# Performance work log

Hardware: AMD Instinct MI355X
Metric: run time of the kernel (lower is better)

Reference implementation:

```python
import jax, jax.numpy as jnp
import numpy as np

# dims: batch B, seq T, model C, expert hidden H, num experts E, top-k K
B, T, C, H, E, K = 4, 1024, 1024, 1024, 8, 2


def _swiglu(x):
    a, b = jnp.split(x, 2, axis=-1)
    return jax.nn.silu(a) * b


def setup_inputs() -> dict:
    key = jax.random.key(0)
    ks = jax.random.split(key, 6)
    s = 0.02
    x = jax.random.normal(ks[0], (B, T, C), jnp.float32)
    # weights stored [in, out] (transpose of torch Linear layout; same math y = x @ W)
    w_shared_in = jax.random.normal(ks[1], (C, 2 * H), jnp.float32) * s
    w_shared_out = jax.random.normal(ks[2], (H, C), jnp.float32) * s
    w1_shared = jax.random.normal(ks[3], (C, 2 * H), jnp.float32) * s
    w2 = jax.random.normal(ks[4], (E, H, C), jnp.float32) * s  # stacked routed_w2
    w_gate = jax.random.normal(ks[5], (C, E), jnp.float32) * s
    gate_bias = jnp.zeros((E,), jnp.float32)  # buffer, updated only in training
    return {
        "x": x,
        "w_shared_in": w_shared_in,
        "w_shared_out": w_shared_out,
        "w1_shared": w1_shared,
        "w2": w2,
        "w_gate": w_gate,
        "gate_bias": gate_bias,
    }


def reference(x, w_shared_in, w_shared_out, w1_shared, w2, w_gate, gate_bias):
    Bx, Tx, Cx = x.shape
    S = Bx * Tx
    fx = x.reshape(S, Cx)  # [S, C]

    # shared expert: SwiGLU MLP
    shared_out = _swiglu(fx @ w_shared_in) @ w_shared_out  # [S, C]

    # router: softmax(top-k) over biased logits
    logits = fx @ w_gate + gate_bias  # [S, E]
    probs = jax.nn.softmax(logits, axis=-1)
    top_val, top_idx = jax.lax.top_k(probs, K)  # [S, K]

    # dense dispatch-weight matrix [S, E] (zero where expert not selected)
    wdense = jnp.zeros((S, E), probs.dtype).at[
        jnp.arange(S)[:, None], top_idx
    ].add(top_val)

    # routed experts share w1_shared, so the SwiGLU hidden is identical for all
    # experts; compute it once for every token, then apply per-expert w2.
    hid = _swiglu(fx @ w1_shared)  # [S, H]
    routed_out = jnp.zeros_like(shared_out)
    for e in range(E):  # small fixed expert count
        routed_out = routed_out + wdense[:, e:e + 1] * (hid @ w2[e])

    return (shared_out + routed_out).reshape(Bx, Tx, Cx)
```

## Files before the change

kernel.cpp:

```cpp
#include <hip/hip_runtime.h>
#include <stdint.h>

typedef __attribute__((ext_vector_type(4))) float f32x4;
typedef __attribute__((ext_vector_type(8))) short s16x8;

static constexpr int S_TOK = 4096;
static constexpr int CDIM  = 1024;
static constexpr int HDIM  = 1024;
static constexpr int H2    = 2048;
static constexpr int NEXP  = 8;

#define BK 32
#define MAXRT2 40

__device__ __forceinline__ unsigned short f2bf(float f) {
  union { float f; uint32_t u; } c; c.f = f;
  uint32_t u = c.u;
  u += 0x7fffu + ((u >> 16) & 1u);
  return (unsigned short)(u >> 16);
}

__device__ __forceinline__ float bf2f(unsigned short u) {
  return __uint_as_float(((uint32_t)u) << 16);
}

__device__ __forceinline__ void gload16(const void* g, void* l) {
  __builtin_amdgcn_global_load_lds(
      (const __attribute__((address_space(1))) void*)g,
      (__attribute__((address_space(3))) void*)l, 16, 0, 0);
}

__global__ void cast_bf16_kernel(const float* __restrict__ src,
                                 unsigned short* __restrict__ dst, int n4) {
  int i = blockIdx.x * blockDim.x + threadIdx.x;
  const int st = gridDim.x * blockDim.x;
  for (; i < n4; i += st) {
    float4 v = reinterpret_cast<const float4*>(src)[i];
    ushort4 o;
    o.x = f2bf(v.x); o.y = f2bf(v.y); o.z = f2bf(v.z); o.w = f2bf(v.w);
    reinterpret_cast<ushort4*>(dst)[i] = o;
  }
}

__global__ void wprep_in_kernel(const float* __restrict__ wsi, const float* __restrict__ w1s,
                                unsigned short* __restrict__ dst) {
  __shared__ float t[32][33];
  const float* src = blockIdx.z ? w1s : wsi;
  const int halfoff = blockIdx.z ? 2048 : 0;
  const int r0 = blockIdx.y * 32;
  const int c0 = blockIdx.x * 32;
  const int tid = threadIdx.x;
#pragma unroll
  for (int i = 0; i < 4; ++i) {
    int idx = tid + i * 256;
    int r = idx >> 5, c = idx & 31;
    t[r][c] = src[(size_t)(r0 + r) * H2 + c0 + c];
  }
  __syncthreads();
#pragma unroll
  for (int i = 0; i < 4; ++i) {
    int idx = tid + i * 256;
    int r = idx >> 5, c = idx & 31;
    const int ccol = c0 + r;
    const int part = ccol >> 10, h = ccol & 1023;
    const int drow = halfoff + (h & 15) + ((h >> 4) << 5) + (part << 4);
    dst[(size_t)drow * CDIM + r0 + c] = f2bf(t[c][r]);
  }
}

__global__ void transpose_cast_kernel(const float* __restrict__ src,
                                      unsigned short* __restrict__ dst,
                                      int R, int Cc) {
  __shared__ float t[32][33];
  const size_t zoff = (size_t)blockIdx.z * R * Cc;
  src += zoff; dst += zoff;
  const int r0 = blockIdx.y * 32;
  const int c0 = blockIdx.x * 32;
  const int tid = threadIdx.x;
#pragma unroll
  for (int i = 0; i < 4; ++i) {
    int idx = tid + i * 256;
    int r = idx >> 5, c = idx & 31;
    t[r][c] = src[(size_t)(r0 + r) * Cc + c0 + c];
  }
  __syncthreads();
#pragma unroll
  for (int i = 0; i < 4; ++i) {
    int idx = tid + i * 256;
    int r = idx >> 5, c = idx & 31;
    dst[(size_t)(c0 + r) * R + r0 + c] = f2bf(t[c][r]);
  }
}

__global__ void router_kernel(const float* __restrict__ x, const float* __restrict__ wg,
                              const float* __restrict__ gb,
                              int2* __restrict__ ti_e, float2* __restrict__ ti_w) {
  const int l = threadIdx.x & 63;
  const int wid = threadIdx.x >> 6;
  const int s = blockIdx.x * 4 + wid;
  const float* xr = x + (size_t)s * CDIM;
  float acc[NEXP];
#pragma unroll
  for (int e = 0; e < NEXP; ++e) acc[e] = 0.f;
  for (int c = l; c < CDIM; c += 64) {
    float xv = xr[c];
    const float* wr_ = wg + (size_t)c * NEXP;
#pragma unroll
    for (int e = 0; e < NEXP; ++e) acc[e] += xv * wr_[e];
  }
#pragma unroll
  for (int e = 0; e < NEXP; ++e) {
#pragma unroll
    for (int off = 32; off > 0; off >>= 1) acc[e] += __shfl_xor(acc[e], off);
    acc[e] += gb[e];
  }
  float m = acc[0];
#pragma unroll
  for (int e = 1; e < NEXP; ++e) m = fmaxf(m, acc[e]);
  float ex[NEXP], sum = 0.f;
#pragma unroll
  for (int e = 0; e < NEXP; ++e) { ex[e] = __expf(acc[e] - m); sum += ex[e]; }
  int i0 = 0;
#pragma unroll
  for (int e = 1; e < NEXP; ++e) if (acc[e] > acc[i0]) i0 = e;
  int i1 = (i0 == 0) ? 1 : 0;
#pragma unroll
  for (int e = 0; e < NEXP; ++e) {
    if (e == i0) continue;
    if (acc[e] > acc[i1]) i1 = e;
  }
  if (l == 0) {
    const float inv = 1.f / sum;
    ti_e[s] = make_int2(i0, i1);
    ti_w[s] = make_float2(ex[i0] * inv, ex[i1] * inv);
  }
}

__global__ __launch_bounds__(1024) void build_kernel(
    const int2* __restrict__ ti_e,
    int* __restrict__ cnt, int* __restrict__ offs,
    int* __restrict__ gidx, int2* __restrict__ ti_slot) {
  __shared__ int gcnt[64][NEXP];
  __shared__ int gbase[64][NEXP];
  __shared__ int eoff[NEXP];
  const int tid = threadIdx.x;
  const int wid = tid >> 6, lane = tid & 63;

  for (int p = 0; p < 4; ++p) {
    const int g = p * 16 + wid;
    const int2 e = ti_e[g * 64 + lane];
#pragma unroll
    for (int ex = 0; ex < NEXP; ++ex) {
      uint64_t b0 = __ballot(e.x == ex);
      uint64_t b1 = __ballot(e.y == ex);
      if (lane == 0) gcnt[g][ex] = __popcll(b0) + __popcll(b1);
    }
  }
  __syncthreads();
  if (tid < NEXP) {
    const int ex = tid;
    int a = 0;
    for (int g = 0; g < 64; ++g) { gbase[g][ex] = a; a += gcnt[g][ex]; }
    eoff[ex] = a;
  }
  __syncthreads();
  if (tid == 0) {
    int a = 0;
#pragma unroll
    for (int ex = 0; ex < NEXP; ++ex) {
      const int c = eoff[ex];
      offs[ex] = a; cnt[ex] = c; eoff[ex] = a; a += c;
    }
    offs[NEXP] = a;
  }
  __syncthreads();
  for (int p = 0; p < 4; ++p) {
    const int g = p * 16 + wid;
    const int s = g * 64 + lane;
    const int2 e = ti_e[s];
    const uint64_t below = (lane == 0) ? 0ull : (~0ull >> (64 - lane));
    const uint64_t beloweq = below | (1ull << lane);
    int slot0 = 0, slot1 = 0;
#pragma unroll
    for (int ex = 0; ex < NEXP; ++ex) {
      uint64_t b0 = __ballot(e.x == ex);
      uint64_t b1 = __ballot(e.y == ex);
      const int base = gbase[g][ex];
      if (e.x == ex) slot0 = base + __popcll(b0 & below) + __popcll(b1 & below);
      if (e.y == ex) slot1 = base + __popcll(b0 & beloweq) + __popcll(b1 & below);
    }
    ti_slot[s] = make_int2(slot0, slot1);
    gidx[eoff[e.x] + slot0] = s;
    gidx[eoff[e.y] + slot1] = s;
  }
}

__global__ __launch_bounds__(256, 4) void gemm1_kernel(
    const unsigned short* __restrict__ xb, const unsigned short* __restrict__ w12i,
    unsigned short* __restrict__ Hs, unsigned short* __restrict__ Hr) {
  __shared__ unsigned short As[128 * BK];
  __shared__ unsigned short Bs[128 * BK];
  const int tid = threadIdx.x;
  const int l = tid & 63, wid = tid >> 6;
  const int wr = wid >> 1, wc = wid & 1;
  const int lr = l & 15, lk = (l >> 4) << 3;
  const int hw = blockIdx.y * gridDim.x + blockIdx.x;
  const int logical = (hw & 7) * 128 + (hw >> 3);
  const int m0 = (logical >> 5) * 128;
  const int n0 = (logical & 31) * 128;
  f32x4 acc[4][4] = {};
  const unsigned short* ga0 = xb + (size_t)(m0 + (tid >> 2)) * CDIM + ((tid & 3) << 3);
  const unsigned short* ga1 = ga0 + (size_t)64 * CDIM;
  const unsigned short* gb0 = w12i + (size_t)(n0 + (tid >> 2)) * CDIM + ((tid & 3) << 3);
  const unsigned short* gb1 = gb0 + (size_t)64 * CDIM;

  for (int k0 = 0; k0 < 1024; k0 += BK) {
    gload16(ga0 + k0, As + tid * 8);
    gload16(ga1 + k0, As + 2048 + tid * 8);
    gload16(gb0 + k0, Bs + tid * 8);
    gload16(gb1 + k0, Bs + 2048 + tid * 8);
    __syncthreads();
    s16x8 a[4], b[4];
#pragma unroll
    for (int fm = 0; fm < 4; ++fm)
      a[fm] = *reinterpret_cast<const s16x8*>(As + (wr * 64 + fm * 16 + lr) * BK + lk);
#pragma unroll
    for (int fn = 0; fn < 4; ++fn)
      b[fn] = *reinterpret_cast<const s16x8*>(Bs + (wc * 64 + fn * 16 + lr) * BK + lk);
#pragma unroll
    for (int fm = 0; fm < 4; ++fm)
#pragma unroll
      for (int fn = 0; fn < 4; ++fn)
        acc[fm][fn] = __builtin_amdgcn_mfma_f32_16x16x32_bf16(a[fm], b[fn], acc[fm][fn], 0, 0, 0);
    __syncthreads();
  }

  unsigned short* Hbuf = (n0 < 2048) ? Hs : Hr;
  const int rb = m0 + wr * 64 + ((l >> 4) << 2);
  const int hb0 = ((n0 & 2047) >> 1) + wc * 32;
#pragma unroll
  for (int fm = 0; fm < 4; ++fm)
#pragma unroll
    for (int j = 0; j < 2; ++j)
#pragma unroll
      for (int r = 0; r < 4; ++r) {
        float a = acc[fm][2 * j][r];
        float b = acc[fm][2 * j + 1][r];
        float hv = (a / (1.f + __expf(-a))) * b;
        Hbuf[(size_t)(rb + fm * 16 + r) * HDIM + hb0 + j * 16 + lr] = f2bf(hv);
      }
}

__global__ __launch_bounds__(512) void gemm2_kernel(
    const unsigned short* __restrict__ Hs, const unsigned short* __restrict__ Hr,
    const unsigned short* __restrict__ wso_t, const unsigned short* __restrict__ w2t,
    const int* __restrict__ cnt, const int* __restrict__ offs, const int* __restrict__ gidx,
    float* __restrict__ out, unsigned short* __restrict__ Eout) {
  __shared__ unsigned short As[2][256 * BK];
  __shared__ unsigned short Bs[2][256 * BK];
  const int tid = threadIdx.x;
  const int l = tid & 63, wid = tid >> 6;
  const int wm = wid >> 2, wn = wid & 3;
  const int lr = l & 15, lk = (l >> 4) << 3;
  const int hw = blockIdx.y * gridDim.x + blockIdx.x;
  const int logical = (hw & 7) * 28 + (hw >> 3);
  const int gx = logical >> 2;
  const int n0 = (logical & 3) * 256;
  f32x4 acc[8][4] = {};

  const int srow = tid >> 2, scol = (tid & 3) << 3;

  const unsigned short* ga0;
  const unsigned short* ga1;
  const unsigned short* gb0;
  const unsigned short* gb1;
  int e = 0, cnte = 0, mt = 0, base = 0;
  const bool dense = (gx < 16);
  if (dense) {
    const int m0 = gx * 256;
    ga0 = Hs + (size_t)(m0 + srow) * HDIM + scol;
    ga1 = ga0 + (size_t)128 * HDIM;
    gb0 = wso_t + (size_t)(n0 + srow) * HDIM + scol;
    gb1 = gb0 + (size_t)128 * HDIM;
  } else {
    int t = gx - 16;
    bool found = false;
#pragma unroll
    for (int ee = 0; ee < NEXP; ++ee) {
      int c = cnt[ee];
      int nt = (c + 255) >> 8;
      if (!found) {
        if (t < nt) { e = ee; cnte = c; found = true; }
        else t -= nt;
      }
    }
    if (!found) return;
    mt = t;
    base = offs[e];
    const int g0 = mt * 256 + srow;
    const int g1 = g0 + 128;
    const int tok0 = gidx[base + min(g0, cnte - 1)];
    const int tok1 = gidx[base + min(g1, cnte - 1)];
    ga0 = Hr + (size_t)tok0 * HDIM + scol;
    ga1 = Hr + (size_t)tok1 * HDIM + scol;
    gb0 = w2t + (size_t)e * CDIM * HDIM + (size_t)(n0 + srow) * HDIM + scol;
    gb1 = gb0 + (size_t)128 * HDIM;
  }

#define STG2(buf, k0) do { \
    gload16(ga0 + (k0), As[buf] + tid * 8); \
    gload16(ga1 + (k0), As[buf] + 4096 + tid * 8); \
    gload16(gb0 + (k0), Bs[buf] + tid * 8); \
    gload16(gb1 + (k0), Bs[buf] + 4096 + tid * 8); \
  } while (0)

  STG2(0, 0);
  asm volatile("s_waitcnt vmcnt(0)" ::: "memory");
  __builtin_amdgcn_s_barrier();
  asm volatile("" ::: "memory");

  const int NT = 1024 / BK;
  for (int t = 0; t < NT; ++t) {
    const int cur = t & 1;
    if (t + 1 < NT) STG2(cur ^ 1, (t + 1) * BK);
    const unsigned short* Ac = As[cur];
    const unsigned short* Bc = Bs[cur];
    s16x8 a[8], b[4];
#pragma unroll
    for (int fm = 0; fm < 8; ++fm)
      a[fm] = *reinterpret_cast<const s16x8*>(Ac + (wm * 128 + fm * 16 + lr) * BK + lk);
#pragma unroll
    for (int fn = 0; fn < 4; ++fn)
      b[fn] = *reinterpret_cast<const s16x8*>(Bc + (wn * 64 + fn * 16 + lr) * BK + lk);
    __builtin_amdgcn_s_setprio(1);
#pragma unroll
    for (int fm = 0; fm < 8; ++fm)
#pragma unroll
      for (int fn = 0; fn < 4; ++fn)
        acc[fm][fn] = __builtin_amdgcn_mfma_f32_16x16x32_bf16(a[fm], b[fn], acc[fm][fn], 0, 0, 0);
    __builtin_amdgcn_s_setprio(0);
    if (t + 1 < NT) {
      asm volatile("s_waitcnt vmcnt(0)" ::: "memory");
      __builtin_amdgcn_s_barrier();
      asm volatile("" ::: "memory");
    }
  }
#undef STG2

  const int rloc0 = wm * 128 + ((l >> 4) << 2);
  const int cb = n0 + wn * 64 + lr;
  if (dense) {
    const int rb = gx * 256 + rloc0;
#pragma unroll
    for (int fm = 0; fm < 8; ++fm)
#pragma unroll
      for (int fn = 0; fn < 4; ++fn)
#pragma unroll
        for (int r = 0; r < 4; ++r)
          out[(size_t)(rb + fm * 16 + r) * CDIM + cb + fn * 16] = acc[fm][fn][r];
  } else {
#pragma unroll
    for (int fm = 0; fm < 8; ++fm)
#pragma unroll
      for (int fn = 0; fn < 4; ++fn)
#pragma unroll
        for (int r = 0; r < 4; ++r) {
          const int rloc = mt * 256 + rloc0 + fm * 16 + r;
          if (rloc < cnte)
            Eout[(size_t)(base + rloc) * CDIM + cb + fn * 16] = f2bf(acc[fm][fn][r]);
        }
  }
}

__global__ void scatter_kernel(float* __restrict__ out, const unsigned short* __restrict__ Eout,
                               const int2* __restrict__ ti_e, const int2* __restrict__ ti_slot,
                               const float2* __restrict__ ti_w, const int* __restrict__ offs) {
  const int total = S_TOK * (CDIM / 8);
  int i = blockIdx.x * blockDim.x + threadIdx.x;
  const int st = gridDim.x * blockDim.x;
  for (; i < total; i += st) {
    const int s = i >> 7;
    const int j = (i & 127) << 3;
    const int2 e = ti_e[s];
    const int2 sl = ti_slot[s];
    const float2 wv = ti_w[s];
    const int p0 = offs[e.x] + sl.x;
    const int p1 = offs[e.y] + sl.y;
    const ushort4* e0 = reinterpret_cast<const ushort4*>(Eout + (size_t)p0 * CDIM + j);
    const ushort4* e1 = reinterpret_cast<const ushort4*>(Eout + (size_t)p1 * CDIM + j);
    float* op = out + (size_t)s * CDIM + j;
#pragma unroll
    for (int q = 0; q < 2; ++q) {
      ushort4 a = e0[q], b = e1[q];
      float4 o = reinterpret_cast<float4*>(op)[q];
      o.x += wv.x * bf2f(a.x) + wv.y * bf2f(b.x);
      o.y += wv.x * bf2f(a.y) + wv.y * bf2f(b.y);
      o.z += wv.x * bf2f(a.z) + wv.y * bf2f(b.z);
      o.w += wv.x * bf2f(a.w) + wv.y * bf2f(b.w);
      reinterpret_cast<float4*>(op)[q] = o;
    }
  }
}

extern "C" void kernel_launch(void* const* d_in, const int* in_sizes, int n_in,
                              void* d_out, int out_size, void* d_ws, size_t ws_size,
                              hipStream_t stream) {
  (void)in_sizes; (void)n_in; (void)out_size; (void)ws_size;
  const float* x   = (const float*)d_in[0];
  const float* wsi = (const float*)d_in[1];
  const float* wso = (const float*)d_in[2];
  const float* w1s = (const float*)d_in[3];
  const float* w2  = (const float*)d_in[4];
  const float* wg  = (const float*)d_in[5];
  const float* gb  = (const float*)d_in[6];
  float* out = (float*)d_out;

  char* w = (char*)d_ws;
  auto alloc = [&](size_t bytes) {
    char* p = w; w += (bytes + 255) & ~(size_t)255; return p;
  };
  unsigned short* xb    = (unsigned short*)alloc((size_t)S_TOK * CDIM * 2);
  unsigned short* w12i  = (unsigned short*)alloc((size_t)2 * H2 * CDIM * 2);
  unsigned short* wso_t = (unsigned short*)alloc((size_t)CDIM * HDIM * 2);
  unsigned short* w2t   = (unsigned short*)alloc((size_t)NEXP * CDIM * HDIM * 2);
  unsigned short* Hs    = (unsigned short*)alloc((size_t)S_TOK * HDIM * 2);
  unsigned short* Hr    = (unsigned short*)alloc((size_t)S_TOK * HDIM * 2);
  unsigned short* Eout  = (unsigned short*)alloc((size_t)2 * S_TOK * CDIM * 2);
  int2*   ti_e   = (int2*)alloc((size_t)S_TOK * 8);
  int2*   ti_slot= (int2*)alloc((size_t)S_TOK * 8);
  float2* ti_w   = (float2*)alloc((size_t)S_TOK * 8);
  int*    cnt    = (int*)alloc(64);
  int*    offs   = (int*)alloc(64);
  int*    gidx   = (int*)alloc((size_t)2 * S_TOK * 4);

  router_kernel<<<S_TOK / 4, 256, 0, stream>>>(x, wg, gb, ti_e, ti_w);
  build_kernel<<<1, 1024, 0, stream>>>(ti_e, cnt, offs, gidx, ti_slot);

  cast_bf16_kernel<<<2048, 256, 0, stream>>>(x, xb, S_TOK * CDIM / 4);
  wprep_in_kernel<<<dim3(H2 / 32, CDIM / 32, 2), 256, 0, stream>>>(wsi, w1s, w12i);
  transpose_cast_kernel<<<dim3(CDIM / 32, HDIM / 32, 1), 256, 0, stream>>>(wso, wso_t, HDIM, CDIM);
  transpose_cast_kernel<<<dim3(CDIM / 32, HDIM / 32, NEXP), 256, 0, stream>>>(w2, w2t, HDIM, CDIM);

  gemm1_kernel<<<dim3(32, 32), 256, 0, stream>>>(xb, w12i, Hs, Hr);

  gemm2_kernel<<<dim3(16 + MAXRT2, CDIM / 256), 512, 0, stream>>>(
      Hs, Hr, wso_t, w2t, cnt, offs, gidx, out, Eout);

  scatter_kernel<<<2048, 256, 0, stream>>>(out, Eout, ti_e, ti_slot, ti_w, offs);
}
```

Baseline: 139.7 us.

## Deepen gemm2 pipeline to 4-stage ring with swizzled LDS and interleaved loads

Replaces gemm2's double-buffered K loop with a 4-slot LDS ring, keeping three stages of global-to-LDS loads in flight and waiting with partial vmcnt counts instead of draining to zero. The per-stage global loads are spread between four MFMA sub-blocks. An XOR swizzle is applied to the LDS column index on both store and read to reduce bank conflicts. The aim is to hide memory latency and cut per-iteration barrier stalls, at the cost of doubling shared memory, which may reduce occupancy.

```diff
diff --git a/kernel.cpp b/kernel.cpp
--- a/kernel.cpp
+++ b/kernel.cpp
@@ -256,32 +256,33 @@
     const unsigned short* __restrict__ wso_t, const unsigned short* __restrict__ w2t,
     const int* __restrict__ cnt, const int* __restrict__ offs, const int* __restrict__ gidx,
     float* __restrict__ out, unsigned short* __restrict__ Eout) {
-  __shared__ unsigned short As[2][256 * BK];
-  __shared__ unsigned short Bs[2][256 * BK];
+  __shared__ unsigned short SA[4][2][4096];
+  __shared__ unsigned short SB[4][2][4096];
   const int tid = threadIdx.x;
   const int l = tid & 63, wid = tid >> 6;
   const int wm = wid >> 2, wn = wid & 3;
-  const int lr = l & 15, lk = (l >> 4) << 3;
+  const int lr = l & 15;
+  const int hi8 = (l >> 4) << 3;
+  const int wnh = wn >> 1;
+  const int wno = (wn & 1) << 6;
   const int hw = blockIdx.y * gridDim.x + blockIdx.x;
   const int logical = (hw & 7) * 28 + (hw >> 3);
   const int gx = logical >> 2;
   const int n0 = (logical & 3) * 256;
   f32x4 acc[8][4] = {};
 
-  const int srow = tid >> 2, scol = (tid & 3) << 3;
-
-  const unsigned short* ga0;
-  const unsigned short* ga1;
-  const unsigned short* gb0;
-  const unsigned short* gb1;
+  const int srow = tid >> 2;
+  const int cs = (((tid & 3) ^ ((tid >> 3) & 3)) << 3);
+
+  const unsigned short *pa0, *pa1, *pb0, *pb1;
   int e = 0, cnte = 0, mt = 0, base = 0;
   const bool dense = (gx < 16);
   if (dense) {
     const int m0 = gx * 256;
-    ga0 = Hs + (size_t)(m0 + srow) * HDIM + scol;
-    ga1 = ga0 + (size_t)128 * HDIM;
-    gb0 = wso_t + (size_t)(n0 + srow) * HDIM + scol;
-    gb1 = gb0 + (size_t)128 * HDIM;
+    pa0 = Hs + (size_t)(m0 + srow) * HDIM + cs;
+    pa1 = pa0 + (size_t)128 * HDIM;
+    pb0 = wso_t + (size_t)(n0 + srow) * HDIM + cs;
+    pb1 = pb0 + (size_t)128 * HDIM;
   } else {
     int t = gx - 16;
     bool found = false;
@@ -297,55 +298,81 @@
     if (!found) return;
     mt = t;
     base = offs[e];
-    const int g0 = mt * 256 + srow;
-    const int g1 = g0 + 128;
-    const int tok0 = gidx[base + min(g0, cnte - 1)];
-    const int tok1 = gidx[base + min(g1, cnte - 1)];
-    ga0 = Hr + (size_t)tok0 * HDIM + scol;
-    ga1 = Hr + (size_t)tok1 * HDIM + scol;
-    gb0 = w2t + (size_t)e * CDIM * HDIM + (size_t)(n0 + srow) * HDIM + scol;
-    gb1 = gb0 + (size_t)128 * HDIM;
-  }
-
-#define STG2(buf, k0) do { \
-    gload16(ga0 + (k0), As[buf] + tid * 8); \
-    gload16(ga1 + (k0), As[buf] + 4096 + tid * 8); \
-    gload16(gb0 + (k0), Bs[buf] + tid * 8); \
-    gload16(gb1 + (k0), Bs[buf] + 4096 + tid * 8); \
-  } while (0)
-
-  STG2(0, 0);
-  asm volatile("s_waitcnt vmcnt(0)" ::: "memory");
-  __builtin_amdgcn_s_barrier();
-  asm volatile("" ::: "memory");
-
-  const int NT = 1024 / BK;
-  for (int t = 0; t < NT; ++t) {
-    const int cur = t & 1;
-    if (t + 1 < NT) STG2(cur ^ 1, (t + 1) * BK);
-    const unsigned short* Ac = As[cur];
-    const unsigned short* Bc = Bs[cur];
+    const int r0 = mt * 256 + srow;
+    const int tok0 = gidx[base + min(r0, cnte - 1)];
+    const int tok1 = gidx[base + min(r0 + 128, cnte - 1)];
+    pa0 = Hr + (size_t)tok0 * HDIM + cs;
+    pa1 = Hr + (size_t)tok1 * HDIM + cs;
+    pb0 = w2t + (size_t)e * CDIM * HDIM + (size_t)(n0 + srow) * HDIM + cs;
+    pb1 = pb0 + (size_t)128 * HDIM;
+  }
+
+  const int t8 = tid * 8;
+#pragma unroll
+  for (int s = 0; s < 3; ++s) {
+    const int kk = s * 32;
+    gload16(pa0 + kk, &SA[s][0][t8]);
+    gload16(pa1 + kk, &SA[s][1][t8]);
+    gload16(pb0 + kk, &SB[s][0][t8]);
+    gload16(pb1 + kk, &SB[s][1][t8]);
+  }
+
+  for (int s = 0; s < 32; ++s) {
+    if (s < 30)       asm volatile("s_waitcnt vmcnt(8)" ::: "memory");
+    else if (s == 30) asm volatile("s_waitcnt vmcnt(4)" ::: "memory");
+    else              asm volatile("s_waitcnt vmcnt(0)" ::: "memory");
+    __builtin_amdgcn_s_barrier();
+    asm volatile("" ::: "memory");
+    const int c = s & 3;
+    const unsigned short* A_ = &SA[c][wm][0];
+    const unsigned short* B_ = &SB[c][wnh][0];
     s16x8 a[8], b[4];
 #pragma unroll
-    for (int fm = 0; fm < 8; ++fm)
-      a[fm] = *reinterpret_cast<const s16x8*>(Ac + (wm * 128 + fm * 16 + lr) * BK + lk);
-#pragma unroll
-    for (int fn = 0; fn < 4; ++fn)
-      b[fn] = *reinterpret_cast<const s16x8*>(Bc + (wn * 64 + fn * 16 + lr) * BK + lk);
+    for (int f = 0; f < 8; ++f) {
+      const int r = f * 16 + lr;
+      a[f] = *reinterpret_cast<const s16x8*>(&A_[r * 32 + (hi8 ^ (((r >> 1) & 3) << 3))]);
+    }
+#pragma unroll
+    for (int j = 0; j < 4; ++j) {
+      const int r = wno + j * 16 + lr;
+      b[j] = *reinterpret_cast<const s16x8*>(&B_[r * 32 + (hi8 ^ (((r >> 1) & 3) << 3))]);
+    }
+    const int c3 = (s + 3) & 3;
+    const int kk = (s + 3) * 32;
+    const bool st = (s <= 28);
+    if (st) gload16(pa0 + kk, &SA[c3][0][t8]);
     __builtin_amdgcn_s_setprio(1);
 #pragma unroll
-    for (int fm = 0; fm < 8; ++fm)
-#pragma unroll
-      for (int fn = 0; fn < 4; ++fn)
-        acc[fm][fn] = __builtin_amdgcn_mfma_f32_16x16x32_bf16(a[fm], b[fn], acc[fm][fn], 0, 0, 0);
+    for (int f = 0; f < 4; ++f) {
+      acc[f][0] = __builtin_amdgcn_mfma_f32_16x16x32_bf16(a[f], b[0], acc[f][0], 0, 0, 0);
+      acc[f][1] = __builtin_amdgcn_mfma_f32_16x16x32_bf16(a[f], b[1], acc[f][1], 0, 0, 0);
+    }
     __builtin_amdgcn_s_setprio(0);
-    if (t + 1 < NT) {
-      asm volatile("s_waitcnt vmcnt(0)" ::: "memory");
-      __builtin_amdgcn_s_barrier();
-      asm volatile("" ::: "memory");
-    }
-  }
-#undef STG2
+    if (st) gload16(pa1 + kk, &SA[c3][1][t8]);
+    __builtin_amdgcn_s_setprio(1);
+#pragma unroll
+    for (int f = 0; f < 4; ++f) {
+      acc[f][2] = __builtin_amdgcn_mfma_f32_16x16x32_bf16(a[f], b[2], acc[f][2], 0, 0, 0);
+      acc[f][3] = __builtin_amdgcn_mfma_f32_16x16x32_bf16(a[f], b[3], acc[f][3], 0, 0, 0);
+    }
+    __builtin_amdgcn_s_setprio(0);
+    if (st) gload16(pb0 + kk, &SB[c3][0][t8]);
+    __builtin_amdgcn_s_setprio(1);
+#pragma unroll
+    for (int f = 0; f < 4; ++f) {
+      acc[4 + f][0] = __builtin_amdgcn_mfma_f32_16x16x32_bf16(a[4 + f], b[0], acc[4 + f][0], 0, 0, 0);
+      acc[4 + f][1] = __builtin_amdgcn_mfma_f32_16x16x32_bf16(a[4 + f], b[1], acc[4 + f][1], 0, 0, 0);
+    }
+    __builtin_amdgcn_s_setprio(0);
+    if (st) gload16(pb1 + kk, &SB[c3][1][t8]);
+    __builtin_amdgcn_s_setprio(1);
+#pragma unroll
+    for (int f = 0; f < 4; ++f) {
+      acc[4 + f][2] = __builtin_amdgcn_mfma_f32_16x16x32_bf16(a[4 + f], b[2], acc[4 + f][2], 0, 0, 0);
+      acc[4 + f][3] = __builtin_amdgcn_mfma_f32_16x16x32_bf16(a[4 + f], b[3], acc[4 + f][3], 0, 0, 0);
+    }
+    __builtin_amdgcn_s_setprio(0);
+  }
 
   const int rloc0 = wm * 128 + ((l >> 4) << 2);
   const int cb = n0 + wn * 64 + lr;
```

Result: faster. 128.7 us (-7.9%).
